# Optimization experiments

Hardware: AMD Instinct MI355X
Metric: run time of the kernel (lower is better)

The kernel has to match this reference:

```python
import jax, jax.numpy as jnp
import numpy as np

NEG_INF = -1e9  # matches torch masked_fill value of -1000000000.0


def setup_inputs() -> dict:
    key = jax.random.key(0)
    k1, k2, k3, k4 = jax.random.split(key, 4)
    B, H, S, D = 4, 16, 2048, 128
    query = jax.random.normal(k1, (B, H, S, D), dtype=jnp.float32)
    key_t = jax.random.normal(k2, (B, H, S, D), dtype=jnp.float32)
    value = jax.random.normal(k3, (B, H, S, D), dtype=jnp.float32)
    mask = jax.random.randint(k4, (B, 1, 1, S), 0, 2, dtype=jnp.int32)
    return {"query": query, "key": key_t, "value": value, "mask": mask, "dropout": 0}


def reference(query, key, value, mask, dropout):
    # scores = Q K^T / sqrt(d_k)   [B,H,S,S]
    d_k = query.shape[-1]
    scores = jnp.einsum("bhqd,bhkd->bhqk", query, key) / jnp.sqrt(jnp.asarray(d_k, query.dtype))
    # masked_fill_(mask == 0, -1e9); mask broadcasts [B,1,1,S] -> [B,H,S,S]
    scores = jnp.where(mask == 0, jnp.asarray(NEG_INF, scores.dtype), scores)
    # dropout == 0 -> identity (deterministic reference / eval mode)
    attn = jax.nn.softmax(scores, axis=-1)
    return jnp.einsum("bhqk,bhkd->bhqd", attn, value)
```

## Files before the change

kernel.cpp:

```cpp
#include <hip/hip_runtime.h>
#include <hip/hip_bf16.h>

#define S_LEN 2048
#define D_DIM 128
#define QBLK 128
#define KVBLK 64
#define NT (S_LEN / KVBLK)
#define KCHUNK 16384
#define VCHUNK 16384
#define PRE_BYTES ((size_t)64 * NT * (KCHUNK + VCHUNK))

typedef __attribute__((ext_vector_type(8))) short short8v;
typedef __attribute__((ext_vector_type(16))) float f32x16;

static __device__ __forceinline__ unsigned f2bf2(float lo, float hi) {
    float2 f2; f2.x = lo; f2.y = hi;
    __hip_bfloat162 h2 = __float22bfloat162_rn(f2);
    unsigned r;
    __builtin_memcpy(&r, &h2, 4);
    return r;
}

static __device__ __forceinline__ void gload16(const void* g, void* l) {
    __builtin_amdgcn_global_load_lds(
        (const __attribute__((address_space(1))) unsigned int*)g,
        (__attribute__((address_space(3))) unsigned int*)l,
        16, 0, 0);
}

static __device__ __forceinline__ void stage16k(const unsigned char* g, unsigned char* l,
                                                int wv, int lane) {
#pragma unroll
    for (int i = 0; i < 4; ++i) {
        const int off = (wv * 4 + i) * 1024;
        gload16(g + off + lane * 16, l + off);
    }
}

#define VTS 133

__global__ __launch_bounds__(256) void preconv(
    const float* __restrict__ Kp, const float* __restrict__ Vp,
    unsigned short* __restrict__ Ko, unsigned short* __restrict__ Vo)
{
    __shared__ float vt[64 * VTS];
    const int tid = threadIdx.x;
    const int blk = blockIdx.x;
    const size_t gbase = (size_t)(blk >> 5) * S_LEN * D_DIM + (size_t)(blk & 31) * KVBLK * D_DIM;

#pragma unroll
    for (int i = 0; i < 8; ++i) {
        int idx = (tid + 256 * i) * 4;
        int row = idx >> 7, col = idx & 127;
        float4 v4 = *(const float4*)(Vp + gbase + idx);
        float* d = &vt[row * VTS + col];
        d[0] = v4.x; d[1] = v4.y; d[2] = v4.z; d[3] = v4.w;
    }

    unsigned short* kout = Ko + (size_t)blk * 8192;
#pragma unroll
    for (int i = 0; i < 4; ++i) {
        int o = tid + 256 * i;
        int row = o >> 4, bs = o & 15;
        int b = (bs & 8) | ((bs ^ row) & 7);
        const float* gp = Kp + gbase + row * D_DIM + 8 * b;
        float4 x = *(const float4*)gp;
        float4 y = *(const float4*)(gp + 4);
        uint4 w;
        w.x = f2bf2(x.x, x.y); w.y = f2bf2(x.z, x.w);
        w.z = f2bf2(y.x, y.y); w.w = f2bf2(y.z, y.w);
        *(uint4*)(kout + o * 8) = w;
    }
    __syncthreads();

    unsigned short* vout = Vo + (size_t)blk * 8192;
#pragma unroll
    for (int i = 0; i < 4; ++i) {
        int o = tid + 256 * i;
        int d = o >> 3, bs = o & 7;
        int b = (bs ^ d) & 7;
        const float* c0 = &vt[(8 * b) * VTS + d];
        uint4 w;
        w.x = f2bf2(c0[0 * VTS], c0[1 * VTS]);
        w.y = f2bf2(c0[2 * VTS], c0[3 * VTS]);
        w.z = f2bf2(c0[4 * VTS], c0[5 * VTS]);
        w.w = f2bf2(c0[6 * VTS], c0[7 * VTS]);
        *(uint4*)(vout + o * 8) = w;
    }
}

#define ASMEM (32768 + 32768 + 8192)

__global__ __launch_bounds__(256, 2) void sdpa_fwd_pre(
    const float* __restrict__ Qp, const unsigned short* __restrict__ Kpre,
    const unsigned short* __restrict__ Vpre, const int* __restrict__ Mp,
    float* __restrict__ Op)
{
    extern __shared__ unsigned char smem[];
    unsigned char* KbB = smem;
    unsigned char* VbB = smem + 32768;
    float* mlds = (float*)(smem + 65536);

    const int tid  = threadIdx.x;
    const int lane = tid & 63;
    const int wv   = tid >> 6;
    const int h    = lane >> 5;
    const int c31  = lane & 31;
    const int hrx  = h ^ (c31 & 7);
    const int lbid = ((blockIdx.x & 7) << 7) | (blockIdx.x >> 3);
    const int bh   = lbid >> 4;
    const int q0   = (lbid & 15) * QBLK;
    const int bb   = bh >> 4;
    const size_t base = (size_t)bh * S_LEN * D_DIM;
    const unsigned char* Kg = (const unsigned char*)Kpre + (size_t)bh * (NT * KCHUNK);
    const unsigned char* Vg = (const unsigned char*)Vpre + (size_t)bh * (NT * VCHUNK);

    constexpr float SC   = 0.08838834764831845f * 1.4426950408889634f;
    constexpr float NEGB = -1.4426950408889634e9f;
    constexpr float THR  = 11.541560327111708f;

    {
        const int* mp = Mp + bb * S_LEN;
#pragma unroll
        for (int i = 0; i < S_LEN / 256; ++i)
            mlds[tid + 256 * i] = mp[tid + 256 * i] ? 0.f : NEGB;
    }

    short8v qf[8];
    {
        const float* qrp = Qp + base + (size_t)(q0 + 32 * wv + c31) * D_DIM;
#pragma unroll
        for (int kk = 0; kk < 8; ++kk) {
            float4 x = *(const float4*)(qrp + 16 * kk + 8 * h);
            float4 y = *(const float4*)(qrp + 16 * kk + 8 * h + 4);
            uint4 w;
            w.x = f2bf2(x.x, x.y); w.y = f2bf2(x.z, x.w);
            w.z = f2bf2(y.x, y.y); w.w = f2bf2(y.z, y.w);
            *(uint4*)&qf[kk] = w;
        }
    }

    stage16k(Kg, KbB, wv, lane);
    stage16k(Vg, VbB, wv, lane);
    __syncthreads();

    f32x16 acc[4];
#pragma unroll
    for (int dt = 0; dt < 4; ++dt)
#pragma unroll
        for (int i = 0; i < 16; ++i) acc[dt][i] = 0.f;

    float m2 = -INFINITY;
    float lsum = 0.f;
    int cur = 0;

#pragma unroll 1
    for (int t0 = 0; t0 < NT; ++t0) {
        const int kv0 = t0 * KVBLK;
        const unsigned char* KcB = KbB + cur * KCHUNK;
        const unsigned char* VcB = VbB + cur * VCHUNK;

        if (t0 + 1 < NT) {
            stage16k(Kg + (size_t)(t0 + 1) * KCHUNK, KbB + (cur ^ 1) * KCHUNK, wv, lane);
            stage16k(Vg + (size_t)(t0 + 1) * VCHUNK, VbB + (cur ^ 1) * VCHUNK, wv, lane);
        }

        f32x16 stc[2];
        __builtin_amdgcn_s_setprio(1);
#pragma unroll
        for (int c = 0; c < 2; ++c) {
            f32x16 s;
#pragma unroll
            for (int i = 0; i < 16; ++i) s[i] = 0.f;
            const unsigned char* rowp = KcB + ((32 * c + c31) << 8);
#pragma unroll
            for (int kk = 0; kk < 8; ++kk) {
                const int bs = ((2 * kk) & 8) | (((2 * kk) & 7) ^ hrx);
                short8v kf = *(const short8v*)(rowp + (bs << 4));
                s = __builtin_amdgcn_mfma_f32_32x32x16_bf16(kf, qf[kk], s, 0, 0, 0);
            }
            stc[c] = s;
        }
        __builtin_amdgcn_s_setprio(0);

        float p[2][16];
#pragma unroll
        for (int c = 0; c < 2; ++c)
#pragma unroll
            for (int t = 0; t < 4; ++t) {
                float4 b4 = *(const float4*)&mlds[kv0 + 32 * c + 8 * t + 4 * h];
                p[c][4 * t + 0] = fmaf(stc[c][4 * t + 0], SC, b4.x);
                p[c][4 * t + 1] = fmaf(stc[c][4 * t + 1], SC, b4.y);
                p[c][4 * t + 2] = fmaf(stc[c][4 * t + 2], SC, b4.z);
                p[c][4 * t + 3] = fmaf(stc[c][4 * t + 3], SC, b4.w);
            }

        float pmax = -INFINITY;
#pragma unroll
        for (int c = 0; c < 2; ++c)
#pragma unroll
            for (int r = 0; r < 16; ++r) pmax = fmaxf(pmax, p[c][r]);
        pmax = fmaxf(pmax, __shfl_xor(pmax, 32));
        if (!__all(pmax <= m2 + THR)) {
            float mnew = fmaxf(m2, pmax);
            float fr = __builtin_amdgcn_exp2f(m2 - mnew);
            m2 = mnew;
            lsum *= fr;
#pragma unroll
            for (int dt = 0; dt < 4; ++dt)
#pragma unroll
                for (int i = 0; i < 16; ++i) acc[dt][i] *= fr;
        }
        float ssum = 0.f;
#pragma unroll
        for (int c = 0; c < 2; ++c)
#pragma unroll
            for (int r = 0; r < 16; ++r) {
                float e = __builtin_amdgcn_exp2f(p[c][r] - m2);
                p[c][r] = e; ssum += e;
            }
        ssum += __shfl_xor(ssum, 32);
        lsum += ssum;

        unsigned w0[2][4], w1[2][4];
#pragma unroll
        for (int c = 0; c < 2; ++c)
#pragma unroll
            for (int t = 0; t < 4; ++t) {
                w0[c][t] = f2bf2(p[c][4 * t + 0], p[c][4 * t + 1]);
                w1[c][t] = f2bf2(p[c][4 * t + 2], p[c][4 * t + 3]);
            }

        __builtin_amdgcn_s_setprio(1);
#pragma unroll
        for (int kk = 0; kk < 4; ++kk) {
            const int t0i = (2 * kk) & 3,     c0i = (2 * kk) >> 2;
            const int t1i = (2 * kk + 1) & 3, c1i = (2 * kk + 1) >> 2;
            unsigned own0 = h ? w0[c1i][t1i] : w0[c0i][t0i];
            unsigned own1 = h ? w1[c1i][t1i] : w1[c0i][t0i];
            unsigned snd0 = h ? w0[c0i][t0i] : w0[c1i][t1i];
            unsigned snd1 = h ? w1[c0i][t0i] : w1[c1i][t1i];
            unsigned r0 = __shfl_xor(snd0, 32);
            unsigned r1 = __shfl_xor(snd1, 32);
            uint4 pw;
            pw.x = h ? r0 : own0;  pw.y = h ? r1 : own1;
            pw.z = h ? own0 : r0;  pw.w = h ? own1 : r1;
            short8v pfv = *(short8v*)&pw;
            const int bs = ((2 * kk) ^ hrx) & 7;
#pragma unroll
            for (int dt = 0; dt < 4; ++dt) {
                short8v vf = *(const short8v*)(VcB + ((32 * dt + c31) << 7) + (bs << 4));
                acc[dt] = __builtin_amdgcn_mfma_f32_32x32x16_bf16(vf, pfv, acc[dt], 0, 0, 0);
            }
        }
        __builtin_amdgcn_s_setprio(0);

        __syncthreads();
        cur ^= 1;
    }

    const float linv = 1.0f / lsum;
    float* sw = (float*)(smem + wv * (32 * 68 * 4));
#pragma unroll
    for (int ph = 0; ph < 2; ++ph) {
#pragma unroll
        for (int dp = 0; dp < 2; ++dp) {
            const int dtg = 2 * ph + dp;
#pragma unroll
            for (int r = 0; r < 16; ++r) {
                int dloc = 32 * dp + (r & 3) + 8 * (r >> 2) + 4 * h;
                sw[c31 * 68 + dloc] = acc[dtg][r] * linv;
            }
        }
#pragma unroll
        for (int it = 0; it < 8; ++it) {
            int f4 = lane + 64 * it;
            int qq = f4 >> 4, c4 = f4 & 15;
            float4 val = *(const float4*)&sw[qq * 68 + 4 * c4];
            *(float4*)(Op + base + (size_t)(q0 + 32 * wv + qq) * D_DIM + 64 * ph + 4 * c4) = val;
        }
    }
}

#define KSTRIDE 136
#define VSTRIDE 72
#define KELEMS (KVBLK * KSTRIDE)
#define VELEMS (D_DIM * VSTRIDE)
#define KBYTES (2 * KELEMS * 2)
#define VBYTES (2 * VELEMS * 2)
#define FBSMEM (KBYTES + VBYTES + S_LEN * 4)

struct KReg { float4 a[4][2]; };
struct VReg { float4 a[2][4]; };

static __device__ __forceinline__ void load_K(KReg& kr, const float* Kbase,
                                              int kv0, int kr0, int kc8) {
#pragma unroll
    for (int i = 0; i < 4; ++i) {
        const float* gp = Kbase + (size_t)(kv0 + kr0 + 16 * i) * D_DIM + 8 * kc8;
        kr.a[i][0] = *(const float4*)gp;
        kr.a[i][1] = *(const float4*)(gp + 4);
    }
}
static __device__ __forceinline__ void write_K(const KReg& kr, unsigned short* Kn,
                                               int kr0, int kc8) {
#pragma unroll
    for (int i = 0; i < 4; ++i) {
        uint4 w;
        w.x = f2bf2(kr.a[i][0].x, kr.a[i][0].y);
        w.y = f2bf2(kr.a[i][0].z, kr.a[i][0].w);
        w.z = f2bf2(kr.a[i][1].x, kr.a[i][1].y);
        w.w = f2bf2(kr.a[i][1].z, kr.a[i][1].w);
        *(uint4*)&Kn[(kr0 + 16 * i) * KSTRIDE + 8 * kc8] = w;
    }
}
static __device__ __forceinline__ void load_V(VReg& vr, const float* Vbase,
                                              int kv0, int vkq, int vdg) {
#pragma unroll
    for (int ii = 0; ii < 2; ++ii)
#pragma unroll
        for (int r = 0; r < 4; ++r)
            vr.a[ii][r] = *(const float4*)(Vbase + (size_t)(kv0 + 4 * vkq + 32 * ii + r) * D_DIM + 4 * vdg);
}
static __device__ __forceinline__ void write_V(const VReg& vr, unsigned short* Vn,
                                               int vkq, int vdg) {
#pragma unroll
    for (int ii = 0; ii < 2; ++ii) {
        const int kvb = 4 * vkq + 32 * ii;
        const int d0  = 4 * vdg;
        uint2 u;
        u.x = f2bf2(vr.a[ii][0].x, vr.a[ii][1].x); u.y = f2bf2(vr.a[ii][2].x, vr.a[ii][3].x);
        *(uint2*)&Vn[(d0 + 0) * VSTRIDE + kvb] = u;
        u.x = f2bf2(vr.a[ii][0].y, vr.a[ii][1].y); u.y = f2bf2(vr.a[ii][2].y, vr.a[ii][3].y);
        *(uint2*)&Vn[(d0 + 1) * VSTRIDE + kvb] = u;
        u.x = f2bf2(vr.a[ii][0].z, vr.a[ii][1].z); u.y = f2bf2(vr.a[ii][2].z, vr.a[ii][3].z);
        *(uint2*)&Vn[(d0 + 2) * VSTRIDE + kvb] = u;
        u.x = f2bf2(vr.a[ii][0].w, vr.a[ii][1].w); u.y = f2bf2(vr.a[ii][2].w, vr.a[ii][3].w);
        *(uint2*)&Vn[(d0 + 3) * VSTRIDE + kvb] = u;
    }
}

__global__ __launch_bounds__(256, 2) void sdpa_fwd_fb(
    const float* __restrict__ Qp, const float* __restrict__ Kp,
    const float* __restrict__ Vp, const int* __restrict__ Mp,
    float* __restrict__ Op)
{
    extern __shared__ unsigned char smem[];
    unsigned short* Kb   = (unsigned short*)smem;
    unsigned short* Vb   = (unsigned short*)(smem + KBYTES);
    float*          mlds = (float*)(smem + KBYTES + VBYTES);

    const int tid  = threadIdx.x;
    const int lane = tid & 63;
    const int wv   = tid >> 6;
    const int h    = lane >> 5;
    const int c31  = lane & 31;
    const int bid  = blockIdx.x;
    const int bh   = bid >> 4;
    const int q0   = (bid & 15) * QBLK;
    const int bb   = bh >> 4;
    const size_t base = (size_t)bh * S_LEN * D_DIM;

    constexpr float SC   = 0.08838834764831845f * 1.4426950408889634f;
    constexpr float NEGB = -1.4426950408889634e9f;
    constexpr float THR  = 11.541560327111708f;

    {
        const int* mp = Mp + bb * S_LEN;
#pragma unroll
        for (int i = 0; i < S_LEN / 256; ++i)
            mlds[tid + 256 * i] = mp[tid + 256 * i] ? 0.f : NEGB;
    }

    short8v qf[8];
    {
        const float* qrp = Qp + base + (size_t)(q0 + 32 * wv + c31) * D_DIM;
#pragma unroll
        for (int kk = 0; kk < 8; ++kk) {
            float4 x = *(const float4*)(qrp + 16 * kk + 8 * h);
            float4 y = *(const float4*)(qrp + 16 * kk + 8 * h + 4);
            uint4 w;
            w.x = f2bf2(x.x, x.y); w.y = f2bf2(x.z, x.w);
            w.z = f2bf2(y.x, y.y); w.w = f2bf2(y.z, y.w);
            *(uint4*)&qf[kk] = w;
        }
    }

    const int kc8 = tid & 15;
    const int kr0 = tid >> 4;
    const int vdg = tid & 31;
    const int vkq = tid >> 5;

    {
        KReg kr; VReg vr;
        load_K(kr, Kp + base, 0, kr0, kc8);
        load_V(vr, Vp + base, 0, vkq, vdg);
        write_K(kr, Kb, kr0, kc8);
        write_V(vr, Vb, vkq, vdg);
    }
    __syncthreads();

    f32x16 acc[4];
#pragma unroll
    for (int dt = 0; dt < 4; ++dt)
#pragma unroll
        for (int i = 0; i < 16; ++i) acc[dt][i] = 0.f;

    float m2 = -INFINITY;
    float lsum = 0.f;
    int cur = 0;

#pragma unroll 1
    for (int t0 = 0; t0 < NT; ++t0) {
        const int kv0 = t0 * KVBLK;
        unsigned short* Kc = Kb + cur * KELEMS;
        unsigned short* Vc = Vb + cur * VELEMS;
        unsigned short* Kn = Kb + (cur ^ 1) * KELEMS;
        unsigned short* Vn = Vb + (cur ^ 1) * VELEMS;
        const bool pf = (t0 + 1 < NT);

        KReg kr; VReg vr;
        if (pf) {
            load_K(kr, Kp + base, kv0 + KVBLK, kr0, kc8);
            load_V(vr, Vp + base, kv0 + KVBLK, vkq, vdg);
        }

        f32x16 stc[2];
        __builtin_amdgcn_s_setprio(1);
#pragma unroll
        for (int c = 0; c < 2; ++c) {
            f32x16 s;
#pragma unroll
            for (int i = 0; i < 16; ++i) s[i] = 0.f;
#pragma unroll
            for (int kk = 0; kk < 8; ++kk) {
                short8v kf = *(const short8v*)&Kc[(32 * c + c31) * KSTRIDE + 16 * kk + 8 * h];
                s = __builtin_amdgcn_mfma_f32_32x32x16_bf16(kf, qf[kk], s, 0, 0, 0);
            }
            stc[c] = s;
        }
        __builtin_amdgcn_s_setprio(0);

        float p[2][16];
#pragma unroll
        for (int c = 0; c < 2; ++c)
#pragma unroll
            for (int t = 0; t < 4; ++t) {
                float4 b4 = *(const float4*)&mlds[kv0 + 32 * c + 8 * t + 4 * h];
                p[c][4 * t + 0] = fmaf(stc[c][4 * t + 0], SC, b4.x);
                p[c][4 * t + 1] = fmaf(stc[c][4 * t + 1], SC, b4.y);
                p[c][4 * t + 2] = fmaf(stc[c][4 * t + 2], SC, b4.z);
                p[c][4 * t + 3] = fmaf(stc[c][4 * t + 3], SC, b4.w);
            }

        float pmax = -INFINITY;
#pragma unroll
        for (int c = 0; c < 2; ++c)
#pragma unroll
            for (int r = 0; r < 16; ++r) pmax = fmaxf(pmax, p[c][r]);
        pmax = fmaxf(pmax, __shfl_xor(pmax, 32));
        if (!__all(pmax <= m2 + THR)) {
            float mnew = fmaxf(m2, pmax);
            float fr = __builtin_amdgcn_exp2f(m2 - mnew);
            m2 = mnew;
            lsum *= fr;
#pragma unroll
            for (int dt = 0; dt < 4; ++dt)
#pragma unroll
                for (int i = 0; i < 16; ++i) acc[dt][i] *= fr;
        }
        float ssum = 0.f;
#pragma unroll
        for (int c = 0; c < 2; ++c)
#pragma unroll
            for (int r = 0; r < 16; ++r) {
                float e = __builtin_amdgcn_exp2f(p[c][r] - m2);
                p[c][r] = e; ssum += e;
            }
        ssum += __shfl_xor(ssum, 32);
        lsum += ssum;

        unsigned w0[2][4], w1[2][4];
#pragma unroll
        for (int c = 0; c < 2; ++c)
#pragma unroll
            for (int t = 0; t < 4; ++t) {
                w0[c][t] = f2bf2(p[c][4 * t + 0], p[c][4 * t + 1]);
                w1[c][t] = f2bf2(p[c][4 * t + 2], p[c][4 * t + 3]);
            }

        __builtin_amdgcn_s_setprio(1);
#pragma unroll
        for (int kk = 0; kk < 4; ++kk) {
            const int t0i = (2 * kk) & 3,     c0i = (2 * kk) >> 2;
            const int t1i = (2 * kk + 1) & 3, c1i = (2 * kk + 1) >> 2;
            unsigned own0 = h ? w0[c1i][t1i] : w0[c0i][t0i];
            unsigned own1 = h ? w1[c1i][t1i] : w1[c0i][t0i];
            unsigned snd0 = h ? w0[c0i][t0i] : w0[c1i][t1i];
            unsigned snd1 = h ? w1[c0i][t0i] : w1[c1i][t1i];
            unsigned r0 = __shfl_xor(snd0, 32);
            unsigned r1 = __shfl_xor(snd1, 32);
            uint4 pw;
            pw.x = h ? r0 : own0;  pw.y = h ? r1 : own1;
            pw.z = h ? own0 : r0;  pw.w = h ? own1 : r1;
            short8v pfv = *(short8v*)&pw;
#pragma unroll
            for (int dt = 0; dt < 4; ++dt) {
                short8v vf = *(const short8v*)&Vc[(32 * dt + c31) * VSTRIDE + 16 * kk + 8 * h];
                acc[dt] = __builtin_amdgcn_mfma_f32_32x32x16_bf16(vf, pfv, acc[dt], 0, 0, 0);
            }
        }
        __builtin_amdgcn_s_setprio(0);

        if (pf) {
            write_K(kr, Kn, kr0, kc8);
            write_V(vr, Vn, vkq, vdg);
        }
        __syncthreads();
        cur ^= 1;
    }

    __syncthreads();
    const float linv = 1.0f / lsum;
    float* sw = (float*)(smem + wv * (32 * 68 * 4));
#pragma unroll
    for (int ph = 0; ph < 2; ++ph) {
#pragma unroll
        for (int dp = 0; dp < 2; ++dp) {
            const int dtg = 2 * ph + dp;
#pragma unroll
            for (int r = 0; r < 16; ++r) {
                int dloc = 32 * dp + (r & 3) + 8 * (r >> 2) + 4 * h;
                sw[c31 * 68 + dloc] = acc[dtg][r] * linv;
            }
        }
#pragma unroll
        for (int it = 0; it < 8; ++it) {
            int f4 = lane + 64 * it;
            int qq = f4 >> 4, c4 = f4 & 15;
            float4 val = *(const float4*)&sw[qq * 68 + 4 * c4];
            *(float4*)(Op + base + (size_t)(q0 + 32 * wv + qq) * D_DIM + 64 * ph + 4 * c4) = val;
        }
    }
}

extern "C" void kernel_launch(void* const* d_in, const int* in_sizes, int n_in,
                              void* d_out, int out_size, void* d_ws, size_t ws_size,
                              hipStream_t stream) {
    (void)in_sizes; (void)n_in; (void)out_size;
    const float* Q = (const float*)d_in[0];
    const float* K = (const float*)d_in[1];
    const float* V = (const float*)d_in[2];
    const int*   M = (const int*)d_in[3];
    float*       O = (float*)d_out;

    if (ws_size >= PRE_BYTES) {
        unsigned short* Kpre = (unsigned short*)d_ws;
        unsigned short* Vpre = (unsigned short*)((char*)d_ws + PRE_BYTES / 2);
        hipLaunchKernelGGL(preconv, dim3(64 * NT), dim3(256), 0, stream, K, V, Kpre, Vpre);
        hipLaunchKernelGGL(sdpa_fwd_pre, dim3(1024), dim3(256), ASMEM, stream, Q, Kpre, Vpre, M, O);
    } else {
        hipLaunchKernelGGL(sdpa_fwd_fb, dim3(1024), dim3(256), FBSMEM, stream, Q, K, V, M, O);
    }
}
```

Before: 209.8 us.

## Halve KV tile, raise occupancy, bitmask mask and fold scale into Q

The KV tile drops from 64 to 32 rows, which halves LDS staging to about 36KB and lets the launch bounds ask for three blocks per CU instead of two. The softmax scale is folded into Q before its bf16 conversion. The additive float mask is replaced by a packed 16-bit bitmask that is ANDed onto the bf16 probabilities after exp, and the row sum is taken from the masked bf16 values. Cross-half reductions and the P operand exchange now use permlane32_swap instead of shuffles, and the preconv V layout is re-swizzled for 32-row chunks. The cost is twice as many loop iterations, each followed by a barrier, plus a changed rounding point for the scale and sum.

```diff
diff --git a/kernel.cpp b/kernel.cpp
--- a/kernel.cpp
+++ b/kernel.cpp
@@ -4,10 +4,10 @@
 #define S_LEN 2048
 #define D_DIM 128
 #define QBLK 128
-#define KVBLK 64
+#define KVBLK 32
 #define NT (S_LEN / KVBLK)
-#define KCHUNK 16384
-#define VCHUNK 16384
+#define KCHUNK 8192
+#define VCHUNK 8192
 #define PRE_BYTES ((size_t)64 * NT * (KCHUNK + VCHUNK))
 
 typedef __attribute__((ext_vector_type(8))) short short8v;
@@ -21,6 +21,21 @@
     return r;
 }
 
+static __device__ __forceinline__ void plswap(unsigned& a, unsigned& b) {
+    auto r = __builtin_amdgcn_permlane32_swap(a, b, false, false);
+    a = r[0]; b = r[1];
+}
+static __device__ __forceinline__ float plswap_max(float x) {
+    unsigned a = __float_as_uint(x), b = a;
+    plswap(a, b);
+    return fmaxf(__uint_as_float(a), __uint_as_float(b));
+}
+static __device__ __forceinline__ float plswap_sum(float x) {
+    unsigned a = __float_as_uint(x), b = a;
+    plswap(a, b);
+    return __uint_as_float(a) + __uint_as_float(b);
+}
+
 static __device__ __forceinline__ void gload16(const void* g, void* l) {
     __builtin_amdgcn_global_load_lds(
         (const __attribute__((address_space(1))) unsigned int*)g,
@@ -28,11 +43,11 @@
         16, 0, 0);
 }
 
-static __device__ __forceinline__ void stage16k(const unsigned char* g, unsigned char* l,
-                                                int wv, int lane) {
-#pragma unroll
-    for (int i = 0; i < 4; ++i) {
-        const int off = (wv * 4 + i) * 1024;
+static __device__ __forceinline__ void stage8k(const unsigned char* g, unsigned char* l,
+                                               int wv, int lane) {
+#pragma unroll
+    for (int i = 0; i < 2; ++i) {
+        const int off = (wv * 2 + i) * 1024;
         gload16(g + off + lane * 16, l + off);
     }
 }
@@ -46,7 +61,7 @@
     __shared__ float vt[64 * VTS];
     const int tid = threadIdx.x;
     const int blk = blockIdx.x;
-    const size_t gbase = (size_t)(blk >> 5) * S_LEN * D_DIM + (size_t)(blk & 31) * KVBLK * D_DIM;
+    const size_t gbase = (size_t)(blk >> 5) * S_LEN * D_DIM + (size_t)(blk & 31) * 64 * D_DIM;
 
 #pragma unroll
     for (int i = 0; i < 8; ++i) {
@@ -76,30 +91,31 @@
     unsigned short* vout = Vo + (size_t)blk * 8192;
 #pragma unroll
     for (int i = 0; i < 4; ++i) {
-        int o = tid + 256 * i;
-        int d = o >> 3, bs = o & 7;
-        int b = (bs ^ d) & 7;
-        const float* c0 = &vt[(8 * b) * VTS + d];
+        int u = tid + 256 * i;
+        int ch = u >> 9, r = u & 511;
+        int d = r >> 2, bs = r & 3;
+        int b = bs ^ ((d >> 1) & 3);
+        const float* c0 = &vt[(ch * 32 + 8 * b) * VTS + d];
         uint4 w;
         w.x = f2bf2(c0[0 * VTS], c0[1 * VTS]);
         w.y = f2bf2(c0[2 * VTS], c0[3 * VTS]);
         w.z = f2bf2(c0[4 * VTS], c0[5 * VTS]);
         w.w = f2bf2(c0[6 * VTS], c0[7 * VTS]);
-        *(uint4*)(vout + o * 8) = w;
-    }
-}
-
-#define ASMEM (32768 + 32768 + 8192)
-
-__global__ __launch_bounds__(256, 2) void sdpa_fwd_pre(
+        *(uint4*)(vout + u * 8) = w;
+    }
+}
+
+#define ASMEM (16384 + 16384 + 4096)
+
+__global__ __launch_bounds__(256, 3) void sdpa_fwd_pre(
     const float* __restrict__ Qp, const unsigned short* __restrict__ Kpre,
     const unsigned short* __restrict__ Vpre, const int* __restrict__ Mp,
     float* __restrict__ Op)
 {
     extern __shared__ unsigned char smem[];
     unsigned char* KbB = smem;
-    unsigned char* VbB = smem + 32768;
-    float* mlds = (float*)(smem + 65536);
+    unsigned char* VbB = smem + 16384;
+    unsigned*      pml = (unsigned*)(smem + 32768);
 
     const int tid  = threadIdx.x;
     const int lane = tid & 63;
@@ -107,6 +123,7 @@
     const int h    = lane >> 5;
     const int c31  = lane & 31;
     const int hrx  = h ^ (c31 & 7);
+    const int vsx  = (c31 >> 1) & 3;
     const int lbid = ((blockIdx.x & 7) << 7) | (blockIdx.x >> 3);
     const int bh   = lbid >> 4;
     const int q0   = (lbid & 15) * QBLK;
@@ -115,6 +132,233 @@
     const unsigned char* Kg = (const unsigned char*)Kpre + (size_t)bh * (NT * KCHUNK);
     const unsigned char* Vg = (const unsigned char*)Vpre + (size_t)bh * (NT * VCHUNK);
 
+    constexpr float SC  = 0.08838834764831845f * 1.4426950408889634f;
+    constexpr float THR = 11.541560327111708f;
+
+    {
+        const int* mp = Mp + bb * S_LEN;
+#pragma unroll
+        for (int i = 0; i < 4; ++i) {
+            int j = tid + 256 * i;
+            int2 mm = *(const int2*)(mp + 2 * j);
+            pml[j] = (mm.x ? 0xFFFFu : 0u) | (mm.y ? 0xFFFF0000u : 0u);
+        }
+    }
+
+    short8v qf[8];
+    {
+        const float* qrp = Qp + base + (size_t)(q0 + 32 * wv + c31) * D_DIM;
+#pragma unroll
+        for (int kk = 0; kk < 8; ++kk) {
+            float4 x = *(const float4*)(qrp + 16 * kk + 8 * h);
+            float4 y = *(const float4*)(qrp + 16 * kk + 8 * h + 4);
+            uint4 w;
+            w.x = f2bf2(x.x * SC, x.y * SC); w.y = f2bf2(x.z * SC, x.w * SC);
+            w.z = f2bf2(y.x * SC, y.y * SC); w.w = f2bf2(y.z * SC, y.w * SC);
+            *(uint4*)&qf[kk] = w;
+        }
+    }
+
+    stage8k(Kg, KbB, wv, lane);
+    stage8k(Vg, VbB, wv, lane);
+    __syncthreads();
+
+    f32x16 acc[4];
+#pragma unroll
+    for (int dt = 0; dt < 4; ++dt)
+#pragma unroll
+        for (int i = 0; i < 16; ++i) acc[dt][i] = 0.f;
+
+    float m2 = -INFINITY;
+    float lsum = 0.f;
+    int cur = 0;
+
+#pragma unroll 1
+    for (int t0 = 0; t0 < NT; ++t0) {
+        const unsigned char* KcB = KbB + cur * KCHUNK;
+        const unsigned char* VcB = VbB + cur * VCHUNK;
+
+        if (t0 + 1 < NT) {
+            stage8k(Kg + (size_t)(t0 + 1) * KCHUNK, KbB + (cur ^ 1) * KCHUNK, wv, lane);
+            stage8k(Vg + (size_t)(t0 + 1) * VCHUNK, VbB + (cur ^ 1) * VCHUNK, wv, lane);
+        }
+
+        f32x16 s;
+#pragma unroll
+        for (int i = 0; i < 16; ++i) s[i] = 0.f;
+        __builtin_amdgcn_s_setprio(1);
+        {
+            const unsigned char* rowp = KcB + (c31 << 8);
+#pragma unroll
+            for (int kk = 0; kk < 8; ++kk) {
+                const int bs = ((2 * kk) & 8) | (((2 * kk) & 7) ^ hrx);
+                short8v kf = *(const short8v*)(rowp + (bs << 4));
+                s = __builtin_amdgcn_mfma_f32_32x32x16_bf16(kf, qf[kk], s, 0, 0, 0);
+            }
+        }
+        __builtin_amdgcn_s_setprio(0);
+
+        float pmax = s[0];
+#pragma unroll
+        for (int r = 1; r < 16; ++r) pmax = fmaxf(pmax, s[r]);
+        pmax = plswap_max(pmax);
+        if (!__all(pmax <= m2 + THR)) {
+            float mnew = fmaxf(m2, pmax);
+            float fr = __builtin_amdgcn_exp2f(m2 - mnew);
+            m2 = mnew;
+            lsum *= fr;
+#pragma unroll
+            for (int dt = 0; dt < 4; ++dt)
+#pragma unroll
+                for (int i = 0; i < 16; ++i) acc[dt][i] *= fr;
+        }
+
+        const unsigned* pmb = pml + ((t0 * KVBLK) >> 1) + 2 * h;
+        unsigned w0[4], w1[4];
+        float ssum = 0.f;
+#pragma unroll
+        for (int t4 = 0; t4 < 4; ++t4) {
+            unsigned pmx = pmb[4 * t4];
+            unsigned pmy = pmb[4 * t4 + 1];
+            float e0 = __builtin_amdgcn_exp2f(s[4 * t4 + 0] - m2);
+            float e1 = __builtin_amdgcn_exp2f(s[4 * t4 + 1] - m2);
+            float e2 = __builtin_amdgcn_exp2f(s[4 * t4 + 2] - m2);
+            float e3 = __builtin_amdgcn_exp2f(s[4 * t4 + 3] - m2);
+            unsigned a = f2bf2(e0, e1) & pmx;
+            unsigned b = f2bf2(e2, e3) & pmy;
+            w0[t4] = a; w1[t4] = b;
+            ssum += __uint_as_float(a << 16) + __uint_as_float(a & 0xFFFF0000u)
+                  + __uint_as_float(b << 16) + __uint_as_float(b & 0xFFFF0000u);
+        }
+        lsum += plswap_sum(ssum);
+
+        __builtin_amdgcn_s_setprio(1);
+#pragma unroll
+        for (int kk = 0; kk < 2; ++kk) {
+            unsigned ax = w0[2 * kk], bx = w0[2 * kk + 1];
+            plswap(ax, bx);
+            unsigned ay = w1[2 * kk], by = w1[2 * kk + 1];
+            plswap(ay, by);
+            uint4 pw;
+            pw.x = ax; pw.y = ay; pw.z = bx; pw.w = by;
+            short8v pfv = *(short8v*)&pw;
+            const int bs = (2 * kk + h) ^ vsx;
+#pragma unroll
+            for (int dt = 0; dt < 4; ++dt) {
+                short8v vf = *(const short8v*)(VcB + ((32 * dt + c31) << 6) + (bs << 4));
+                acc[dt] = __builtin_amdgcn_mfma_f32_32x32x16_bf16(vf, pfv, acc[dt], 0, 0, 0);
+            }
+        }
+        __builtin_amdgcn_s_setprio(0);
+
+        __syncthreads();
+        cur ^= 1;
+    }
+
+    const float linv = 1.0f / lsum;
+    float* sw = (float*)(smem + wv * (32 * 68 * 4));
+#pragma unroll
+    for (int ph = 0; ph < 2; ++ph) {
+#pragma unroll
+        for (int dp = 0; dp < 2; ++dp) {
+            const int dtg = 2 * ph + dp;
+#pragma unroll
+            for (int r = 0; r < 16; ++r) {
+                int dloc = 32 * dp + (r & 3) + 8 * (r >> 2) + 4 * h;
+                sw[c31 * 68 + dloc] = acc[dtg][r] * linv;
+            }
+        }
+#pragma unroll
+        for (int it = 0; it < 8; ++it) {
+            int f4 = lane + 64 * it;
+            int qq = f4 >> 4, c4 = f4 & 15;
+            float4 val = *(const float4*)&sw[qq * 68 + 4 * c4];
+            *(float4*)(Op + base + (size_t)(q0 + 32 * wv + qq) * D_DIM + 64 * ph + 4 * c4) = val;
+        }
+    }
+}
+
+#define FBKV 64
+#define FBNT (S_LEN / FBKV)
+#define KSTRIDE 136
+#define VSTRIDE 72
+#define KELEMS (FBKV * KSTRIDE)
+#define VELEMS (D_DIM * VSTRIDE)
+#define KBYTES (2 * KELEMS * 2)
+#define VBYTES (2 * VELEMS * 2)
+#define FBSMEM (KBYTES + VBYTES + S_LEN * 4)
+
+struct KReg { float4 a[4][2]; };
+struct VReg { float4 a[2][4]; };
+
+static __device__ __forceinline__ void load_K(KReg& kr, const float* Kbase,
+                                              int kv0, int kr0, int kc8) {
+#pragma unroll
+    for (int i = 0; i < 4; ++i) {
+        const float* gp = Kbase + (size_t)(kv0 + kr0 + 16 * i) * D_DIM + 8 * kc8;
+        kr.a[i][0] = *(const float4*)gp;
+        kr.a[i][1] = *(const float4*)(gp + 4);
+    }
+}
+static __device__ __forceinline__ void write_K(const KReg& kr, unsigned short* Kn,
+                                               int kr0, int kc8) {
+#pragma unroll
+    for (int i = 0; i < 4; ++i) {
+        uint4 w;
+        w.x = f2bf2(kr.a[i][0].x, kr.a[i][0].y);
+        w.y = f2bf2(kr.a[i][0].z, kr.a[i][0].w);
+        w.z = f2bf2(kr.a[i][1].x, kr.a[i][1].y);
+        w.w = f2bf2(kr.a[i][1].z, kr.a[i][1].w);
+        *(uint4*)&Kn[(kr0 + 16 * i) * KSTRIDE + 8 * kc8] = w;
+    }
+}
+static __device__ __forceinline__ void load_V(VReg& vr, const float* Vbase,
+                                              int kv0, int vkq, int vdg) {
+#pragma unroll
+    for (int ii = 0; ii < 2; ++ii)
+#pragma unroll
+        for (int r = 0; r < 4; ++r)
+            vr.a[ii][r] = *(const float4*)(Vbase + (size_t)(kv0 + 4 * vkq + 32 * ii + r) * D_DIM + 4 * vdg);
+}
+static __device__ __forceinline__ void write_V(const VReg& vr, unsigned short* Vn,
+                                               int vkq, int vdg) {
+#pragma unroll
+    for (int ii = 0; ii < 2; ++ii) {
+        const int kvb = 4 * vkq + 32 * ii;
+        const int d0  = 4 * vdg;
+        uint2 u;
+        u.x = f2bf2(vr.a[ii][0].x, vr.a[ii][1].x); u.y = f2bf2(vr.a[ii][2].x, vr.a[ii][3].x);
+        *(uint2*)&Vn[(d0 + 0) * VSTRIDE + kvb] = u;
+        u.x = f2bf2(vr.a[ii][0].y, vr.a[ii][1].y); u.y = f2bf2(vr.a[ii][2].y, vr.a[ii][3].y);
+        *(uint2*)&Vn[(d0 + 1) * VSTRIDE + kvb] = u;
+        u.x = f2bf2(vr.a[ii][0].z, vr.a[ii][1].z); u.y = f2bf2(vr.a[ii][2].z, vr.a[ii][3].z);
+        *(uint2*)&Vn[(d0 + 2) * VSTRIDE + kvb] = u;
+        u.x = f2bf2(vr.a[ii][0].w, vr.a[ii][1].w); u.y = f2bf2(vr.a[ii][2].w, vr.a[ii][3].w);
+        *(uint2*)&Vn[(d0 + 3) * VSTRIDE + kvb] = u;
+    }
+}
+
+__global__ __launch_bounds__(256, 2) void sdpa_fwd_fb(
+    const float* __restrict__ Qp, const float* __restrict__ Kp,
+    const float* __restrict__ Vp, const int* __restrict__ Mp,
+    float* __restrict__ Op)
+{
+    extern __shared__ unsigned char smem[];
+    unsigned short* Kb   = (unsigned short*)smem;
+    unsigned short* Vb   = (unsigned short*)(smem + KBYTES);
+    float*          mlds = (float*)(smem + KBYTES + VBYTES);
+
+    const int tid  = threadIdx.x;
+    const int lane = tid & 63;
+    const int wv   = tid >> 6;
+    const int h    = lane >> 5;
+    const int c31  = lane & 31;
+    const int bid  = blockIdx.x;
+    const int bh   = bid >> 4;
+    const int q0   = (bid & 15) * QBLK;
+    const int bb   = bh >> 4;
+    const size_t base = (size_t)bh * S_LEN * D_DIM;
+
     constexpr float SC   = 0.08838834764831845f * 1.4426950408889634f;
     constexpr float NEGB = -1.4426950408889634e9f;
     constexpr float THR  = 11.541560327111708f;
@@ -140,8 +384,18 @@
         }
     }
 
-    stage16k(Kg, KbB, wv, lane);
-    stage16k(Vg, VbB, wv, lane);
+    const int kc8 = tid & 15;
+    const int kr0 = tid >> 4;
+    const int vdg = tid & 31;
+    const int vkq = tid >> 5;
+
+    {
+        KReg kr; VReg vr;
+        load_K(kr, Kp + base, 0, kr0, kc8);
+        load_V(vr, Vp + base, 0, vkq, vdg);
+        write_K(kr, Kb, kr0, kc8);
+        write_V(vr, Vb, vkq, vdg);
+    }
     __syncthreads();
 
     f32x16 acc[4];
@@ -155,14 +409,18 @@
     int cur = 0;
 
 #pragma unroll 1
-    for (int t0 = 0; t0 < NT; ++t0) {
-        const int kv0 = t0 * KVBLK;
-        const unsigned char* KcB = KbB + cur * KCHUNK;
-        const unsigned char* VcB = VbB + cur * VCHUNK;
-
-        if (t0 + 1 < NT) {
-            stage16k(Kg + (size_t)(t0 + 1) * KCHUNK, KbB + (cur ^ 1) * KCHUNK, wv, lane);
-            stage16k(Vg + (size_t)(t0 + 1) * VCHUNK, VbB + (cur ^ 1) * VCHUNK, wv, lane);
+    for (int t0 = 0; t0 < FBNT; ++t0) {
+        const int kv0 = t0 * FBKV;
+        unsigned short* Kc = Kb + cur * KELEMS;
+        unsigned short* Vc = Vb + cur * VELEMS;
+        unsigned short* Kn = Kb + (cur ^ 1) * KELEMS;
+        unsigned short* Vn = Vb + (cur ^ 1) * VELEMS;
+        const bool pf = (t0 + 1 < FBNT);
+
+        KReg kr; VReg vr;
+        if (pf) {
+            load_K(kr, Kp + base, kv0 + FBKV, kr0, kc8);
+            load_V(vr, Vp + base, kv0 + FBKV, vkq, vdg);
         }
 
         f32x16 stc[2];
@@ -172,11 +430,9 @@
             f32x16 s;
 #pragma unroll
             for (int i = 0; i < 16; ++i) s[i] = 0.f;
-            const unsigned char* rowp = KcB + ((32 * c + c31) << 8);
 #pragma unroll
             for (int kk = 0; kk < 8; ++kk) {
-                const int bs = ((2 * kk) & 8) | (((2 * kk) & 7) ^ hrx);
-                short8v kf = *(const short8v*)(rowp + (bs << 4));
+                short8v kf = *(const short8v*)&Kc[(32 * c + c31) * KSTRIDE + 16 * kk + 8 * h];
                 s = __builtin_amdgcn_mfma_f32_32x32x16_bf16(kf, qf[kk], s, 0, 0, 0);
             }
             stc[c] = s;
@@ -246,264 +502,6 @@
             pw.x = h ? r0 : own0;  pw.y = h ? r1 : own1;
             pw.z = h ? own0 : r0;  pw.w = h ? own1 : r1;
             short8v pfv = *(short8v*)&pw;
-            const int bs = ((2 * kk) ^ hrx) & 7;
-#pragma unroll
-            for (int dt = 0; dt < 4; ++dt) {
-                short8v vf = *(const short8v*)(VcB + ((32 * dt + c31) << 7) + (bs << 4));
-                acc[dt] = __builtin_amdgcn_mfma_f32_32x32x16_bf16(vf, pfv, acc[dt], 0, 0, 0);
-            }
-        }
-        __builtin_amdgcn_s_setprio(0);
-
-        __syncthreads();
-        cur ^= 1;
-    }
-
-    const float linv = 1.0f / lsum;
-    float* sw = (float*)(smem + wv * (32 * 68 * 4));
-#pragma unroll
-    for (int ph = 0; ph < 2; ++ph) {
-#pragma unroll
-        for (int dp = 0; dp < 2; ++dp) {
-            const int dtg = 2 * ph + dp;
-#pragma unroll
-            for (int r = 0; r < 16; ++r) {
-                int dloc = 32 * dp + (r & 3) + 8 * (r >> 2) + 4 * h;
-                sw[c31 * 68 + dloc] = acc[dtg][r] * linv;
-            }
-        }
-#pragma unroll
-        for (int it = 0; it < 8; ++it) {
-            int f4 = lane + 64 * it;
-            int qq = f4 >> 4, c4 = f4 & 15;
-            float4 val = *(const float4*)&sw[qq * 68 + 4 * c4];
-            *(float4*)(Op + base + (size_t)(q0 + 32 * wv + qq) * D_DIM + 64 * ph + 4 * c4) = val;
-        }
-    }
-}
-
-#define KSTRIDE 136
-#define VSTRIDE 72
-#define KELEMS (KVBLK * KSTRIDE)
-#define VELEMS (D_DIM * VSTRIDE)
-#define KBYTES (2 * KELEMS * 2)
-#define VBYTES (2 * VELEMS * 2)
-#define FBSMEM (KBYTES + VBYTES + S_LEN * 4)
-
-struct KReg { float4 a[4][2]; };
-struct VReg { float4 a[2][4]; };
-
-static __device__ __forceinline__ void load_K(KReg& kr, const float* Kbase,
-                                              int kv0, int kr0, int kc8) {
-#pragma unroll
-    for (int i = 0; i < 4; ++i) {
-        const float* gp = Kbase + (size_t)(kv0 + kr0 + 16 * i) * D_DIM + 8 * kc8;
-        kr.a[i][0] = *(const float4*)gp;
-        kr.a[i][1] = *(const float4*)(gp + 4);
-    }
-}
-static __device__ __forceinline__ void write_K(const KReg& kr, unsigned short* Kn,
-                                               int kr0, int kc8) {
-#pragma unroll
-    for (int i = 0; i < 4; ++i) {
-        uint4 w;
-        w.x = f2bf2(kr.a[i][0].x, kr.a[i][0].y);
-        w.y = f2bf2(kr.a[i][0].z, kr.a[i][0].w);
-        w.z = f2bf2(kr.a[i][1].x, kr.a[i][1].y);
-        w.w = f2bf2(kr.a[i][1].z, kr.a[i][1].w);
-        *(uint4*)&Kn[(kr0 + 16 * i) * KSTRIDE + 8 * kc8] = w;
-    }
-}
-static __device__ __forceinline__ void load_V(VReg& vr, const float* Vbase,
-                                              int kv0, int vkq, int vdg) {
-#pragma unroll
-    for (int ii = 0; ii < 2; ++ii)
-#pragma unroll
-        for (int r = 0; r < 4; ++r)
-            vr.a[ii][r] = *(const float4*)(Vbase + (size_t)(kv0 + 4 * vkq + 32 * ii + r) * D_DIM + 4 * vdg);
-}
-static __device__ __forceinline__ void write_V(const VReg& vr, unsigned short* Vn,
-                                               int vkq, int vdg) {
-#pragma unroll
-    for (int ii = 0; ii < 2; ++ii) {
-        const int kvb = 4 * vkq + 32 * ii;
-        const int d0  = 4 * vdg;
-        uint2 u;
-        u.x = f2bf2(vr.a[ii][0].x, vr.a[ii][1].x); u.y = f2bf2(vr.a[ii][2].x, vr.a[ii][3].x);
-        *(uint2*)&Vn[(d0 + 0) * VSTRIDE + kvb] = u;
-        u.x = f2bf2(vr.a[ii][0].y, vr.a[ii][1].y); u.y = f2bf2(vr.a[ii][2].y, vr.a[ii][3].y);
-        *(uint2*)&Vn[(d0 + 1) * VSTRIDE + kvb] = u;
-        u.x = f2bf2(vr.a[ii][0].z, vr.a[ii][1].z); u.y = f2bf2(vr.a[ii][2].z, vr.a[ii][3].z);
-        *(uint2*)&Vn[(d0 + 2) * VSTRIDE + kvb] = u;
-        u.x = f2bf2(vr.a[ii][0].w, vr.a[ii][1].w); u.y = f2bf2(vr.a[ii][2].w, vr.a[ii][3].w);
-        *(uint2*)&Vn[(d0 + 3) * VSTRIDE + kvb] = u;
-    }
-}
-
-__global__ __launch_bounds__(256, 2) void sdpa_fwd_fb(
-    const float* __restrict__ Qp, const float* __restrict__ Kp,
-    const float* __restrict__ Vp, const int* __restrict__ Mp,
-    float* __restrict__ Op)
-{
-    extern __shared__ unsigned char smem[];
-    unsigned short* Kb   = (unsigned short*)smem;
-    unsigned short* Vb   = (unsigned short*)(smem + KBYTES);
-    float*          mlds = (float*)(smem + KBYTES + VBYTES);
-
-    const int tid  = threadIdx.x;
-    const int lane = tid & 63;
-    const int wv   = tid >> 6;
-    const int h    = lane >> 5;
-    const int c31  = lane & 31;
-    const int bid  = blockIdx.x;
-    const int bh   = bid >> 4;
-    const int q0   = (bid & 15) * QBLK;
-    const int bb   = bh >> 4;
-    const size_t base = (size_t)bh * S_LEN * D_DIM;
-
-    constexpr float SC   = 0.08838834764831845f * 1.4426950408889634f;
-    constexpr float NEGB = -1.4426950408889634e9f;
-    constexpr float THR  = 11.541560327111708f;
-
-    {
-        const int* mp = Mp + bb * S_LEN;
-#pragma unroll
-        for (int i = 0; i < S_LEN / 256; ++i)
-            mlds[tid + 256 * i] = mp[tid + 256 * i] ? 0.f : NEGB;
-    }
-
-    short8v qf[8];
-    {
-        const float* qrp = Qp + base + (size_t)(q0 + 32 * wv + c31) * D_DIM;
-#pragma unroll
-        for (int kk = 0; kk < 8; ++kk) {
-            float4 x = *(const float4*)(qrp + 16 * kk + 8 * h);
-            float4 y = *(const float4*)(qrp + 16 * kk + 8 * h + 4);
-            uint4 w;
-            w.x = f2bf2(x.x, x.y); w.y = f2bf2(x.z, x.w);
-            w.z = f2bf2(y.x, y.y); w.w = f2bf2(y.z, y.w);
-            *(uint4*)&qf[kk] = w;
-        }
-    }
-
-    const int kc8 = tid & 15;
-    const int kr0 = tid >> 4;
-    const int vdg = tid & 31;
-    const int vkq = tid >> 5;
-
-    {
-        KReg kr; VReg vr;
-        load_K(kr, Kp + base, 0, kr0, kc8);
-        load_V(vr, Vp + base, 0, vkq, vdg);
-        write_K(kr, Kb, kr0, kc8);
-        write_V(vr, Vb, vkq, vdg);
-    }
-    __syncthreads();
-
-    f32x16 acc[4];
-#pragma unroll
-    for (int dt = 0; dt < 4; ++dt)
-#pragma unroll
-        for (int i = 0; i < 16; ++i) acc[dt][i] = 0.f;
-
-    float m2 = -INFINITY;
-    float lsum = 0.f;
-    int cur = 0;
-
-#pragma unroll 1
-    for (int t0 = 0; t0 < NT; ++t0) {
-        const int kv0 = t0 * KVBLK;
-        unsigned short* Kc = Kb + cur * KELEMS;
-        unsigned short* Vc = Vb + cur * VELEMS;
-        unsigned short* Kn = Kb + (cur ^ 1) * KELEMS;
-        unsigned short* Vn = Vb + (cur ^ 1) * VELEMS;
-        const bool pf = (t0 + 1 < NT);
-
-        KReg kr; VReg vr;
-        if (pf) {
-            load_K(kr, Kp + base, kv0 + KVBLK, kr0, kc8);
-            load_V(vr, Vp + base, kv0 + KVBLK, vkq, vdg);
-        }
-
-        f32x16 stc[2];
-        __builtin_amdgcn_s_setprio(1);
-#pragma unroll
-        for (int c = 0; c < 2; ++c) {
-            f32x16 s;
-#pragma unroll
-            for (int i = 0; i < 16; ++i) s[i] = 0.f;
-#pragma unroll
-            for (int kk = 0; kk < 8; ++kk) {
-                short8v kf = *(const short8v*)&Kc[(32 * c + c31) * KSTRIDE + 16 * kk + 8 * h];
-                s = __builtin_amdgcn_mfma_f32_32x32x16_bf16(kf, qf[kk], s, 0, 0, 0);
-            }
-            stc[c] = s;
-        }
-        __builtin_amdgcn_s_setprio(0);
-
-        float p[2][16];
-#pragma unroll
-        for (int c = 0; c < 2; ++c)
-#pragma unroll
-            for (int t = 0; t < 4; ++t) {
-                float4 b4 = *(const float4*)&mlds[kv0 + 32 * c + 8 * t + 4 * h];
-                p[c][4 * t + 0] = fmaf(stc[c][4 * t + 0], SC, b4.x);
-                p[c][4 * t + 1] = fmaf(stc[c][4 * t + 1], SC, b4.y);
-                p[c][4 * t + 2] = fmaf(stc[c][4 * t + 2], SC, b4.z);
-                p[c][4 * t + 3] = fmaf(stc[c][4 * t + 3], SC, b4.w);
-            }
-
-        float pmax = -INFINITY;
-#pragma unroll
-        for (int c = 0; c < 2; ++c)
-#pragma unroll
-            for (int r = 0; r < 16; ++r) pmax = fmaxf(pmax, p[c][r]);
-        pmax = fmaxf(pmax, __shfl_xor(pmax, 32));
-        if (!__all(pmax <= m2 + THR)) {
-            float mnew = fmaxf(m2, pmax);
-            float fr = __builtin_amdgcn_exp2f(m2 - mnew);
-            m2 = mnew;
-            lsum *= fr;
-#pragma unroll
-            for (int dt = 0; dt < 4; ++dt)
-#pragma unroll
-                for (int i = 0; i < 16; ++i) acc[dt][i] *= fr;
-        }
-        float ssum = 0.f;
-#pragma unroll
-        for (int c = 0; c < 2; ++c)
-#pragma unroll
-            for (int r = 0; r < 16; ++r) {
-                float e = __builtin_amdgcn_exp2f(p[c][r] - m2);
-                p[c][r] = e; ssum += e;
-            }
-        ssum += __shfl_xor(ssum, 32);
-        lsum += ssum;
-
-        unsigned w0[2][4], w1[2][4];
-#pragma unroll
-        for (int c = 0; c < 2; ++c)
-#pragma unroll
-            for (int t = 0; t < 4; ++t) {
-                w0[c][t] = f2bf2(p[c][4 * t + 0], p[c][4 * t + 1]);
-                w1[c][t] = f2bf2(p[c][4 * t + 2], p[c][4 * t + 3]);
-            }
-
-        __builtin_amdgcn_s_setprio(1);
-#pragma unroll
-        for (int kk = 0; kk < 4; ++kk) {
-            const int t0i = (2 * kk) & 3,     c0i = (2 * kk) >> 2;
-            const int t1i = (2 * kk + 1) & 3, c1i = (2 * kk + 1) >> 2;
-            unsigned own0 = h ? w0[c1i][t1i] : w0[c0i][t0i];
-            unsigned own1 = h ? w1[c1i][t1i] : w1[c0i][t0i];
-            unsigned snd0 = h ? w0[c0i][t0i] : w0[c1i][t1i];
-            unsigned snd1 = h ? w1[c0i][t0i] : w1[c1i][t1i];
-            unsigned r0 = __shfl_xor(snd0, 32);
-            unsigned r1 = __shfl_xor(snd1, 32);
-            uint4 pw;
-            pw.x = h ? r0 : own0;  pw.y = h ? r1 : own1;
-            pw.z = h ? own0 : r0;  pw.w = h ? own1 : r1;
-            short8v pfv = *(short8v*)&pw;
 #pragma unroll
             for (int dt = 0; dt < 4; ++dt) {
                 short8v vf = *(const short8v*)&Vc[(32 * dt + c31) * VSTRIDE + 16 * kk + 8 * h];
@@ -557,7 +555,7 @@
     if (ws_size >= PRE_BYTES) {
         unsigned short* Kpre = (unsigned short*)d_ws;
         unsigned short* Vpre = (unsigned short*)((char*)d_ws + PRE_BYTES / 2);
-        hipLaunchKernelGGL(preconv, dim3(64 * NT), dim3(256), 0, stream, K, V, Kpre, Vpre);
+        hipLaunchKernelGGL(preconv, dim3(64 * 32), dim3(256), 0, stream, K, V, Kpre, Vpre);
         hipLaunchKernelGGL(sdpa_fwd_pre, dim3(1024), dim3(256), ASMEM, stream, Q, Kpre, Vpre, M, O);
     } else {
         hipLaunchKernelGGL(sdpa_fwd_fb, dim3(1024), dim3(256), FBSMEM, stream, Q, K, V, M, O);
```

Measured after the change: 203.4 us. 1.03x faster.
